# Performance work log

Hardware: AMD Instinct MI355X
Metric: run time of the kernel (lower is better)

Reference implementation:

```python
import jax, jax.numpy as jnp
import numpy as np

BN_EPS = 1e-5


def setup_inputs() -> dict:
    key = jax.random.key(0)
    ks = jax.random.split(key, 8)
    N, E, D, G, L = 50000, 800000, 128, 64, 4
    x = jax.random.normal(ks[0], (N, D), dtype=jnp.float32)
    edge_index = jax.random.randint(ks[1], (2, E), 0, N, dtype=jnp.int64)
    batch = jnp.sort(jax.random.randint(ks[2], (N,), 0, G, dtype=jnp.int64))
    sc = 1.0 / np.sqrt(D)
    W1 = jax.random.normal(ks[3], (L, D, D), dtype=jnp.float32) * sc
    b1 = jnp.zeros((L, D), dtype=jnp.float32)
    gamma = jnp.ones((L, D), dtype=jnp.float32)
    beta = jnp.zeros((L, D), dtype=jnp.float32)
    W2 = jax.random.normal(ks[4], (L, D, D), dtype=jnp.float32) * sc
    b2 = jnp.zeros((L, D), dtype=jnp.float32)
    return {"x": x, "edge_index": edge_index, "batch": batch,
            "W1": W1, "b1": b1, "gamma": gamma, "beta": beta,
            "W2": W2, "b2": b2}


def _segment_mean(vals, ids, num_segments):
    s = jax.ops.segment_sum(vals, ids, num_segments=num_segments)
    cnt = jax.ops.segment_sum(jnp.ones((vals.shape[0],), vals.dtype), ids,
                              num_segments=num_segments)
    return s / jnp.clip(cnt, 1.0)[:, None]


def reference(x, edge_index, batch, W1, b1, gamma, beta, W2, b2):
    N = x.shape[0]
    L = W1.shape[0]
    G = 64  # number of graphs
    src, dst = edge_index[0], edge_index[1]  # source_to_target flow
    # in-degree counts for scatter-mean (fixed across layers)
    deg = jax.ops.segment_sum(jnp.ones((src.shape[0],), x.dtype), dst,
                              num_segments=N)
    deg = jnp.clip(deg, 1.0)[:, None]
    h = x
    node_pool = jnp.zeros((N, W1.shape[2]), x.dtype)
    g_pool = jnp.zeros((G, W1.shape[2]), x.dtype)
    for l in range(L):
        # scatter-mean neighbor aggregation, GIN update with eps=0
        agg = jax.ops.segment_sum(h[src], dst, num_segments=N) / deg
        z = h + agg
        # MLP: Linear -> BatchNorm1d (batch stats) -> ReLU -> Linear
        z = z @ W1[l] + b1[l]
        mu = jnp.mean(z, axis=0)
        var = jnp.mean(jnp.square(z - mu), axis=0)  # biased, as in torch BN
        z = gamma[l] * (z - mu) * jax.lax.rsqrt(var + BN_EPS) + beta[l]
        z = jax.nn.relu(z)
        h = z @ W2[l] + b2[l]
        node_pool = node_pool + h
        g_pool = g_pool + _segment_mean(h, batch, G)
    return node_pool, g_pool
```

## Files before the change

kernel.cpp:

```cpp
#include <hip/hip_runtime.h>

#define D 128
#define GNUM 64
#define LNUM 4
#define BN_EPS 1e-5f
#define EPB 16384
#define SH_MAX 12544

typedef short bf16x8 __attribute__((ext_vector_type(8)));
typedef float f32x4 __attribute__((ext_vector_type(4)));
typedef unsigned short u16x8 __attribute__((ext_vector_type(8)));
typedef unsigned short u16x4 __attribute__((ext_vector_type(4)));

__device__ __forceinline__ float bf2f(unsigned short u) {
  union { unsigned int i; float f; } v; v.i = ((unsigned int)u) << 16; return v.f;
}
__device__ __forceinline__ unsigned short f2bf(float f) {
  union { float f; unsigned int i; } v; v.f = f;
  unsigned int b = v.i;
  return (unsigned short)((b + 0x7FFFu + ((b >> 16) & 1u)) >> 16);
}

__global__ __launch_bounds__(256) void k_hist(const int* __restrict__ ei, int E,
                                              int B, int nbin, int* __restrict__ hist) {
  __shared__ int lh[256];
  int b = blockIdx.x, tx = threadIdx.x;
  lh[tx] = 0;
  __syncthreads();
  int s = b * EPB, e = min(s + EPB, E);
  for (int j = s + tx; j < e; j += 256) atomicAdd(&lh[ei[(size_t)E + j] >> 8], 1);
  __syncthreads();
  if (tx < nbin) hist[tx * B + b] = lh[tx];
}

__global__ __launch_bounds__(1024) void k_hscan(const int* __restrict__ hist, int M,
                                                int* __restrict__ off,
                                                int* __restrict__ rowptr, int N, int E) {
  __shared__ int sh[SH_MAX];
  __shared__ int sh2[1024];
  int tx = threadIdx.x;
  int chunk = (M + 1023) / 1024;
  for (int i = 0; i < chunk; ++i) {
    int idx = tx * chunk + i;
    sh[idx] = (idx < M) ? hist[idx] : 0;
  }
  __syncthreads();
  int s = 0;
  for (int i = 0; i < chunk; ++i) s += sh[tx * chunk + i];
  sh2[tx] = s;
  __syncthreads();
  for (int o = 1; o < 1024; o <<= 1) {
    int u = (tx >= o) ? sh2[tx - o] : 0;
    __syncthreads();
    sh2[tx] += u;
    __syncthreads();
  }
  int run = (tx == 0) ? 0 : sh2[tx - 1];
  for (int i = 0; i < chunk; ++i) {
    int idx = tx * chunk + i;
    if (idx < M) { int v = sh[idx]; off[idx] = run; run += v; }
  }
  if (tx == 0) rowptr[N] = E;
}

__global__ __launch_bounds__(256) void k_scatter(const int* __restrict__ ei, int E,
                                                 int B, int nbin,
                                                 const int* __restrict__ off,
                                                 int2* __restrict__ sorted) {
  __shared__ int cur[256];
  int b = blockIdx.x, tx = threadIdx.x;
  if (tx < nbin) cur[tx] = off[tx * B + b];
  __syncthreads();
  int s = b * EPB, e = min(s + EPB, E);
  for (int j = s + tx; j < e; j += 256) {
    int d = ei[(size_t)E + j];
    int sc = ei[j];
    int p = atomicAdd(&cur[d >> 8], 1);
    sorted[p] = make_int2(d, sc);
  }
}

__global__ __launch_bounds__(256) void k_build(const int2* __restrict__ sorted,
                                               const int* __restrict__ off,
                                               int B, int nbin, int E, int N,
                                               int* __restrict__ rowptr,
                                               int* __restrict__ col) {
  __shared__ int cnt[256], excl[256], cur[256];
  int beta = blockIdx.x, tx = threadIdx.x;
  int s = off[beta * B];
  int e = (beta + 1 < nbin) ? off[(beta + 1) * B] : E;
  cnt[tx] = 0;
  __syncthreads();
  for (int j = s + tx; j < e; j += 256) atomicAdd(&cnt[sorted[j].x & 255], 1);
  __syncthreads();
  int v = cnt[tx];
  excl[tx] = v;
  __syncthreads();
  for (int o = 1; o < 256; o <<= 1) {
    int u = (tx >= o) ? excl[tx - o] : 0;
    __syncthreads();
    excl[tx] += u;
    __syncthreads();
  }
  int ex = excl[tx] - v;
  int n = beta * 256 + tx;
  if (n < N) rowptr[n] = s + ex;
  cur[tx] = s + ex;
  __syncthreads();
  for (int j = s + tx; j < e; j += 256) {
    int2 p = sorted[j];
    int q = atomicAdd(&cur[p.x & 255], 1);
    col[q] = p.y;
  }
}

__global__ void k_bounds(const int* __restrict__ batch, int N, int* __restrict__ bound) {
  int g = threadIdx.x;
  if (g > GNUM) return;
  int lo = 0, hi = N;
  while (lo < hi) { int mid = (lo + hi) >> 1; if (batch[mid] < g) lo = mid + 1; else hi = mid; }
  bound[g] = lo;
}

__global__ void k_prep_x(const float* __restrict__ x, unsigned short* __restrict__ hx, int total4) {
  int i = blockIdx.x * 256 + threadIdx.x;
  if (i < total4) {
    f32x4 v = ((const f32x4*)x)[i];
    u16x4 o; o[0] = f2bf(v[0]); o[1] = f2bf(v[1]); o[2] = f2bf(v[2]); o[3] = f2bf(v[3]);
    ((u16x4*)hx)[i] = o;
  }
}

__global__ __launch_bounds__(256) void k_prep_w(const float* __restrict__ W1,
                                                const float* __restrict__ W2,
                                                unsigned short* __restrict__ wt) {
  int l = blockIdx.x;
  const float* W = (l < LNUM) ? (W1 + (size_t)l * D * D) : (W2 + (size_t)(l - LNUM) * D * D);
  unsigned short* o = wt + (size_t)l * D * D;
#pragma unroll
  for (int i = 0; i < 64; ++i) {
    int idx = threadIdx.x + 256 * i;
    int k = idx >> 7, n = idx & 127;
    o[n * D + k] = f2bf(W[idx]);
  }
}

__global__ __launch_bounds__(256) void k_layer1(const unsigned short* __restrict__ hin,
                                                const int* __restrict__ rowptr,
                                                const int* __restrict__ col,
                                                const unsigned short* __restrict__ wt,
                                                const float* __restrict__ bias,
                                                unsigned short* __restrict__ t,
                                                float* __restrict__ partials, int N) {
  __shared__ union { unsigned short wl[D * D]; float out[64 * D]; } uB;
  __shared__ float red[2 * 8 * D];
  int tx = threadIdx.x;
  int r0 = blockIdx.x * 64;
  const u16x8* wg = (const u16x8*)wt;
#pragma unroll
  for (int i = 0; i < 8; ++i) {
    int cid = tx + 256 * i;
    int row = cid >> 4, c16 = cid & 15;
    u16x8 v = wg[cid];
    *(u16x8*)((char*)uB.wl + row * 256 + ((c16 * 16) ^ ((row & 7) << 4))) = v;
  }
  int l = tx & 63, w = tx >> 6;
  int lm = l & 15, lg = l >> 4;
  int row = 16 * w + lm;
  int n = r0 + row;
  const u16x8* h8 = (const u16x8*)hin;
  f32x4 sA[4] = {{0.f,0.f,0.f,0.f},{0.f,0.f,0.f,0.f},{0.f,0.f,0.f,0.f},{0.f,0.f,0.f,0.f}};
  f32x4 sB[4] = {{0.f,0.f,0.f,0.f},{0.f,0.f,0.f,0.f},{0.f,0.f,0.f,0.f},{0.f,0.f,0.f,0.f}};
  int e0 = 0, e1 = 0;
  if (n < N) { e0 = rowptr[n]; e1 = rowptr[n + 1]; }
  int j = e0;
  for (; j + 1 < e1; j += 2) {
    size_t c0 = (size_t)col[j] * 16 + lg;
    size_t c1 = (size_t)col[j + 1] * 16 + lg;
    u16x8 v00 = h8[c0];      u16x8 v01 = h8[c0 + 4];
    u16x8 v02 = h8[c0 + 8];  u16x8 v03 = h8[c0 + 12];
    u16x8 v10 = h8[c1];      u16x8 v11 = h8[c1 + 4];
    u16x8 v12 = h8[c1 + 8];  u16x8 v13 = h8[c1 + 12];
#pragma unroll
    for (int k = 0; k < 4; ++k) {
      sA[0][k] += bf2f(v00[k]) + bf2f(v10[k]);
      sB[0][k] += bf2f(v00[4 + k]) + bf2f(v10[4 + k]);
      sA[1][k] += bf2f(v01[k]) + bf2f(v11[k]);
      sB[1][k] += bf2f(v01[4 + k]) + bf2f(v11[4 + k]);
      sA[2][k] += bf2f(v02[k]) + bf2f(v12[k]);
      sB[2][k] += bf2f(v02[4 + k]) + bf2f(v12[4 + k]);
      sA[3][k] += bf2f(v03[k]) + bf2f(v13[k]);
      sB[3][k] += bf2f(v03[4 + k]) + bf2f(v13[4 + k]);
    }
  }
  if (j < e1) {
    size_t c0 = (size_t)col[j] * 16 + lg;
    u16x8 v00 = h8[c0];      u16x8 v01 = h8[c0 + 4];
    u16x8 v02 = h8[c0 + 8];  u16x8 v03 = h8[c0 + 12];
#pragma unroll
    for (int k = 0; k < 4; ++k) {
      sA[0][k] += bf2f(v00[k]);  sB[0][k] += bf2f(v00[4 + k]);
      sA[1][k] += bf2f(v01[k]);  sB[1][k] += bf2f(v01[4 + k]);
      sA[2][k] += bf2f(v02[k]);  sB[2][k] += bf2f(v02[4 + k]);
      sA[3][k] += bf2f(v03[k]);  sB[3][k] += bf2f(v03[4 + k]);
    }
  }
  bf16x8 af[4];
  if (n < N) {
    float inv = (e1 > e0) ? 1.f / (float)(e1 - e0) : 0.f;
#pragma unroll
    for (int kt = 0; kt < 4; ++kt) {
      u16x8 hv = h8[(size_t)n * 16 + kt * 4 + lg];
      u16x8 o;
#pragma unroll
      for (int k = 0; k < 4; ++k) {
        o[k] = f2bf(bf2f(hv[k]) + sA[kt][k] * inv);
        o[4 + k] = f2bf(bf2f(hv[4 + k]) + sB[kt][k] * inv);
      }
      af[kt] = *(bf16x8*)&o;
    }
  } else {
#pragma unroll
    for (int kt = 0; kt < 4; ++kt) af[kt] = (bf16x8){0,0,0,0,0,0,0,0};
  }
  __syncthreads();
  f32x4 acc[8];
#pragma unroll
  for (int cc = 0; cc < 8; ++cc) { float bv = bias[cc * 16 + lm]; acc[cc] = (f32x4){bv, bv, bv, bv}; }
#pragma unroll
  for (int kt = 0; kt < 4; ++kt) {
    int koff = kt * 64 + lg * 16;
#pragma unroll
    for (int cc = 0; cc < 8; ++cc) {
      int nn = cc * 16 + lm;
      bf16x8 bfr = *(const bf16x8*)((const char*)uB.wl + nn * 256 + (koff ^ ((nn & 7) << 4)));
      acc[cc] = __builtin_amdgcn_mfma_f32_16x16x32_bf16(af[kt], bfr, acc[cc], 0, 0, 0);
    }
  }
  __syncthreads();
#pragma unroll
  for (int cc = 0; cc < 8; ++cc)
#pragma unroll
    for (int r = 0; r < 4; ++r)
      uB.out[(16 * w + 4 * lg + r) * D + cc * 16 + lm] = acc[cc][r];
  __syncthreads();
  int tc = tx & 31, tr = tx >> 5;
  f32x4 s = {0.f, 0.f, 0.f, 0.f}, q = {0.f, 0.f, 0.f, 0.f};
#pragma unroll
  for (int i = 0; i < 8; ++i) {
    int rr = i * 8 + tr;
    f32x4 v = *(f32x4*)&uB.out[rr * D + tc * 4];
    u16x4 o; o[0] = f2bf(v[0]); o[1] = f2bf(v[1]); o[2] = f2bf(v[2]); o[3] = f2bf(v[3]);
    *(u16x4*)(t + (size_t)(r0 + rr) * D + tc * 4) = o;
    if (r0 + rr < N) { s += v; q += v * v; }
  }
  *(f32x4*)&red[tr * D + tc * 4] = s;
  *(f32x4*)&red[8 * D + tr * D + tc * 4] = q;
  __syncthreads();
  int colx = tx & 127, which = tx >> 7;
  float S = 0.f;
#pragma unroll
  for (int jj = 0; jj < 8; ++jj) S += red[which * 8 * D + jj * D + colx];
  partials[(size_t)blockIdx.x * 256 + tx] = S;
}

__global__ __launch_bounds__(256) void k_red1(const float* __restrict__ partials, int NB,
                                              float* __restrict__ partial2) {
  int tx = threadIdx.x;
  float S = 0.f;
  for (int b = blockIdx.x; b < NB; b += 64) S += partials[(size_t)b * 256 + tx];
  partial2[(size_t)blockIdx.x * 256 + tx] = S;
}

__global__ __launch_bounds__(256) void k_finalize(const float* __restrict__ partial2,
                                                  const float* __restrict__ gamma,
                                                  const float* __restrict__ beta,
                                                  float* __restrict__ stats, int N) {
  __shared__ float sh[256];
  int tx = threadIdx.x;
  float S = 0.f;
#pragma unroll 8
  for (int b = 0; b < 64; ++b) S += partial2[(size_t)b * 256 + tx];
  sh[tx] = S;
  __syncthreads();
  if (tx < D) {
    float mu = sh[tx] / (float)N;
    float var = sh[D + tx] / (float)N - mu * mu;
    float rstd = rsqrtf(fmaxf(var, 0.f) + BN_EPS);
    float A = gamma[tx] * rstd;
    stats[tx] = A;
    stats[D + tx] = beta[tx] - mu * A;
  }
}

__device__ __forceinline__ void gemm2_core(const unsigned short* t,
                                           const unsigned short* wt,
                                           const float* bias, const float* stats,
                                           unsigned short* at, unsigned short* wl,
                                           float* outbuf, int r0) {
  int tx = threadIdx.x;
  const u16x8* tg = (const u16x8*)(t + (size_t)r0 * D);
#pragma unroll
  for (int i = 0; i < 4; ++i) {
    int cid = tx + 256 * i;
    int row = cid >> 4, c16 = cid & 15;
    u16x8 v = tg[cid];
    int c0 = c16 * 8;
    f32x4 a0 = *(const f32x4*)&stats[c0];
    f32x4 a1 = *(const f32x4*)&stats[c0 + 4];
    f32x4 b0 = *(const f32x4*)&stats[D + c0];
    f32x4 b1v = *(const f32x4*)&stats[D + c0 + 4];
    u16x8 o;
    o[0] = f2bf(fmaxf(bf2f(v[0]) * a0[0] + b0[0], 0.f));
    o[1] = f2bf(fmaxf(bf2f(v[1]) * a0[1] + b0[1], 0.f));
    o[2] = f2bf(fmaxf(bf2f(v[2]) * a0[2] + b0[2], 0.f));
    o[3] = f2bf(fmaxf(bf2f(v[3]) * a0[3] + b0[3], 0.f));
    o[4] = f2bf(fmaxf(bf2f(v[4]) * a1[0] + b1v[0], 0.f));
    o[5] = f2bf(fmaxf(bf2f(v[5]) * a1[1] + b1v[1], 0.f));
    o[6] = f2bf(fmaxf(bf2f(v[6]) * a1[2] + b1v[2], 0.f));
    o[7] = f2bf(fmaxf(bf2f(v[7]) * a1[3] + b1v[3], 0.f));
    *(u16x8*)((char*)at + row * 256 + ((c16 * 16) ^ ((row & 7) << 4))) = o;
  }
  const u16x8* wg = (const u16x8*)wt;
#pragma unroll
  for (int i = 0; i < 8; ++i) {
    int cid = tx + 256 * i;
    int row = cid >> 4, c16 = cid & 15;
    u16x8 v = wg[cid];
    *(u16x8*)((char*)wl + row * 256 + ((c16 * 16) ^ ((row & 7) << 4))) = v;
  }
  __syncthreads();
  int l = tx & 63, w = tx >> 6;
  int lm = l & 15, lg = l >> 4;
  f32x4 acc[8];
#pragma unroll
  for (int c = 0; c < 8; ++c) { float bv = bias[c * 16 + lm]; acc[c] = (f32x4){bv, bv, bv, bv}; }
  int arow = 16 * w + lm;
  const char* ab = (const char*)at + arow * 256;
  int aswz = (arow & 7) << 4;
#pragma unroll
  for (int kt = 0; kt < 4; ++kt) {
    int koff = kt * 64 + lg * 16;
    bf16x8 af = *(const bf16x8*)(ab + (koff ^ aswz));
#pragma unroll
    for (int c = 0; c < 8; ++c) {
      int n = c * 16 + lm;
      bf16x8 bfr = *(const bf16x8*)((const char*)wl + n * 256 + (koff ^ ((n & 7) << 4)));
      acc[c] = __builtin_amdgcn_mfma_f32_16x16x32_bf16(af, bfr, acc[c], 0, 0, 0);
    }
  }
  __syncthreads();
#pragma unroll
  for (int c = 0; c < 8; ++c)
#pragma unroll
    for (int r = 0; r < 4; ++r)
      outbuf[(16 * w + 4 * lg + r) * D + c * 16 + lm] = acc[c][r];
  __syncthreads();
}

__global__ __launch_bounds__(256) void k_gemm2(const unsigned short* __restrict__ t,
                                               const unsigned short* __restrict__ wt,
                                               const float* __restrict__ bias,
                                               const float* __restrict__ stats,
                                               unsigned short* __restrict__ h, int N) {
  __shared__ unsigned short at[64 * D];
  __shared__ union { unsigned short wl[D * D]; float out[64 * D]; } uB;
  int tx = threadIdx.x;
  int r0 = blockIdx.x * 64;
  gemm2_core(t, wt, bias, stats, at, uB.wl, uB.out, r0);
  int tc = tx & 31, tr = tx >> 5;
#pragma unroll
  for (int i = 0; i < 8; ++i) {
    int row = i * 8 + tr;
    int gr = r0 + row;
    if (gr < N) {
      f32x4 v = *(f32x4*)&uB.out[row * D + tc * 4];
      u16x4 hb; hb[0] = f2bf(v[0]); hb[1] = f2bf(v[1]); hb[2] = f2bf(v[2]); hb[3] = f2bf(v[3]);
      *(u16x4*)(h + (size_t)gr * D + tc * 4) = hb;
    }
  }
}

__global__ __launch_bounds__(256) void k_gemm2_last(const unsigned short* __restrict__ t,
                                                    const unsigned short* __restrict__ wt,
                                                    const float* __restrict__ bias,
                                                    const float* __restrict__ stats,
                                                    const unsigned short* __restrict__ h0,
                                                    const unsigned short* __restrict__ h1,
                                                    const unsigned short* __restrict__ h2,
                                                    float* __restrict__ np, int N) {
  __shared__ unsigned short at[64 * D];
  __shared__ union { unsigned short wl[D * D]; float out[64 * D]; } uB;
  int tx = threadIdx.x;
  int r0 = blockIdx.x * 64;
  gemm2_core(t, wt, bias, stats, at, uB.wl, uB.out, r0);
  int tc = tx & 31, tr = tx >> 5;
#pragma unroll
  for (int i = 0; i < 8; ++i) {
    int row = i * 8 + tr;
    int gr = r0 + row;
    if (gr < N) {
      f32x4 v = *(f32x4*)&uB.out[row * D + tc * 4];
      size_t o4 = (size_t)gr * D + tc * 4;
      u16x4 a = *(const u16x4*)(h0 + o4);
      u16x4 b = *(const u16x4*)(h1 + o4);
      u16x4 cc = *(const u16x4*)(h2 + o4);
      f32x4 o;
#pragma unroll
      for (int k = 0; k < 4; ++k)
        o[k] = v[k] + (bf2f(a[k]) + bf2f(b[k])) + bf2f(cc[k]);
      *(f32x4*)(np + o4) = o;
    }
  }
}

__global__ __launch_bounds__(256) void k_gpool(const float* __restrict__ np,
                                               const int* __restrict__ bound,
                                               float* __restrict__ gp) {
  __shared__ float red[8 * D];
  int g = blockIdx.x;
  int s = bound[g], e = bound[g + 1];
  int tc = threadIdx.x & 31, tr = threadIdx.x >> 5;
  f32x4 a = {0.f, 0.f, 0.f, 0.f};
  for (int r = s + tr; r < e; r += 8)
    a += *(const f32x4*)(np + (size_t)r * D + tc * 4);
  *(f32x4*)&red[tr * D + tc * 4] = a;
  __syncthreads();
  if (threadIdx.x < D) {
    float v = 0.f;
#pragma unroll
    for (int j = 0; j < 8; ++j) v += red[j * D + threadIdx.x];
    float c = (float)(e - s);
    gp[(size_t)g * D + threadIdx.x] = v / fmaxf(c, 1.f);
  }
}

extern "C" void kernel_launch(void* const* d_in, const int* in_sizes, int n_in,
                              void* d_out, int out_size, void* d_ws,
                              size_t ws_size, hipStream_t stream) {
  const float* x = (const float*)d_in[0];
  const int* ei = (const int*)d_in[1];
  const int* batch = (const int*)d_in[2];
  const float* W1 = (const float*)d_in[3];
  const float* b1 = (const float*)d_in[4];
  const float* gamma = (const float*)d_in[5];
  const float* beta = (const float*)d_in[6];
  const float* W2 = (const float*)d_in[7];
  const float* b2 = (const float*)d_in[8];
  int N = in_sizes[0] / D;
  int E = in_sizes[1] / 2;
  int Npad = (N + 63) & ~63;
  int gb = Npad / 64;
  int B = (E + EPB - 1) / EPB;
  int nbin = (N + 255) / 256;
  int M = nbin * B;

  float* out = (float*)d_out;
  float* node_pool = out;
  float* g_pool = out + (size_t)N * D;

  char* wp = (char*)d_ws;
  unsigned short* hx = (unsigned short*)wp;   wp += (size_t)Npad * D * 2;
  unsigned short* t = (unsigned short*)wp;    wp += (size_t)Npad * D * 2;
  unsigned short* hbuf[3];
  for (int l = 0; l < 3; ++l) { hbuf[l] = (unsigned short*)wp; wp += (size_t)Npad * D * 2; }
  unsigned short* wt = (unsigned short*)wp;   wp += (size_t)8 * D * D * 2;
  float* partials = (float*)wp;               wp += (size_t)gb * 256 * 4;
  float* partial2 = (float*)wp;               wp += (size_t)64 * 256 * 4;
  float* stats = (float*)wp;                  wp += (size_t)2 * D * 4;
  int* bound = (int*)wp;                      wp += (size_t)(GNUM + 4) * 4;
  int* rowptr = (int*)wp;                     wp += (size_t)(N + 1) * 4;
  int* hist = (int*)wp;                       wp += (size_t)SH_MAX * 4;
  int* off = (int*)wp;                        wp += (size_t)SH_MAX * 4;
  int* col = (int*)wp;                        wp += (size_t)E * 4;
  int2* sorted = (int2*)wp;                   wp += (size_t)E * 8;

  k_prep_w<<<8, 256, 0, stream>>>(W1, W2, wt);
  k_prep_x<<<(N * 32 + 255) / 256, 256, 0, stream>>>(x, hx, N * 32);
  k_hist<<<B, 256, 0, stream>>>(ei, E, B, nbin, hist);
  k_hscan<<<1, 1024, 0, stream>>>(hist, M, off, rowptr, N, E);
  k_scatter<<<B, 256, 0, stream>>>(ei, E, B, nbin, off, sorted);
  k_build<<<nbin, 256, 0, stream>>>(sorted, off, B, nbin, E, N, rowptr, col);
  k_bounds<<<1, 128, 0, stream>>>(batch, N, bound);

  for (int ll = 0; ll < LNUM; ++ll) {
    const unsigned short* hin = (ll == 0) ? hx : hbuf[ll - 1];
    k_layer1<<<gb, 256, 0, stream>>>(hin, rowptr, col, wt + (size_t)ll * D * D,
                                     b1 + (size_t)ll * D, t, partials, N);
    k_red1<<<64, 256, 0, stream>>>(partials, gb, partial2);
    k_finalize<<<1, 256, 0, stream>>>(partial2, gamma + (size_t)ll * D,
                                      beta + (size_t)ll * D, stats, N);
    if (ll < LNUM - 1) {
      k_gemm2<<<gb, 256, 0, stream>>>(t, wt + (size_t)(LNUM + ll) * D * D,
                                      b2 + (size_t)ll * D, stats, hbuf[ll], N);
    } else {
      k_gemm2_last<<<gb, 256, 0, stream>>>(t, wt + (size_t)(LNUM + ll) * D * D,
                                           b2 + (size_t)ll * D, stats,
                                           hbuf[0], hbuf[1], hbuf[2], node_pool, N);
    }
  }
  k_gpool<<<GNUM, 256, 0, stream>>>(node_pool, bound, g_pool);
}
```

Baseline: 428.0 us.

## Sort rows by in-degree within each tile to balance gather work across lanes

```diff
diff --git a/kernel.cpp b/kernel.cpp
--- a/kernel.cpp
+++ b/kernel.cpp
@@ -122,6 +122,24 @@
   bound[g] = lo;
 }
 
+__global__ __launch_bounds__(64) void k_perm(const int* __restrict__ rowptr, int N,
+                                             int* __restrict__ perm) {
+  __shared__ int degs[64];
+  int r0 = blockIdx.x * 64;
+  int i = threadIdx.x;
+  int n = r0 + i;
+  int d = (n < N) ? (rowptr[n + 1] - rowptr[n]) : -1;
+  degs[i] = d;
+  __syncthreads();
+  int rank = 0;
+#pragma unroll
+  for (int j = 0; j < 64; ++j) {
+    int dj = degs[j];
+    if (dj < d || (dj == d && j < i)) ++rank;
+  }
+  perm[r0 + rank] = i;
+}
+
 __global__ void k_prep_x(const float* __restrict__ x, unsigned short* __restrict__ hx, int total4) {
   int i = blockIdx.x * 256 + threadIdx.x;
   if (i < total4) {
@@ -148,6 +166,7 @@
 __global__ __launch_bounds__(256) void k_layer1(const unsigned short* __restrict__ hin,
                                                 const int* __restrict__ rowptr,
                                                 const int* __restrict__ col,
+                                                const int* __restrict__ perm,
                                                 const unsigned short* __restrict__ wt,
                                                 const float* __restrict__ bias,
                                                 unsigned short* __restrict__ t,
@@ -166,43 +185,48 @@
   }
   int l = tx & 63, w = tx >> 6;
   int lm = l & 15, lg = l >> 4;
-  int row = 16 * w + lm;
-  int n = r0 + row;
+  int lr = perm[r0 + 16 * w + lm];
+  int pr0 = perm[r0 + 16 * w + 4 * lg + 0];
+  int pr1 = perm[r0 + 16 * w + 4 * lg + 1];
+  int pr2 = perm[r0 + 16 * w + 4 * lg + 2];
+  int pr3 = perm[r0 + 16 * w + 4 * lg + 3];
+  int n = r0 + lr;
   const u16x8* h8 = (const u16x8*)hin;
   f32x4 sA[4] = {{0.f,0.f,0.f,0.f},{0.f,0.f,0.f,0.f},{0.f,0.f,0.f,0.f},{0.f,0.f,0.f,0.f}};
   f32x4 sB[4] = {{0.f,0.f,0.f,0.f},{0.f,0.f,0.f,0.f},{0.f,0.f,0.f,0.f},{0.f,0.f,0.f,0.f}};
   int e0 = 0, e1 = 0;
   if (n < N) { e0 = rowptr[n]; e1 = rowptr[n + 1]; }
   int j = e0;
-  for (; j + 1 < e1; j += 2) {
-    size_t c0 = (size_t)col[j] * 16 + lg;
-    size_t c1 = (size_t)col[j + 1] * 16 + lg;
-    u16x8 v00 = h8[c0];      u16x8 v01 = h8[c0 + 4];
-    u16x8 v02 = h8[c0 + 8];  u16x8 v03 = h8[c0 + 12];
-    u16x8 v10 = h8[c1];      u16x8 v11 = h8[c1 + 4];
-    u16x8 v12 = h8[c1 + 8];  u16x8 v13 = h8[c1 + 12];
+  for (; j + 3 < e1; j += 4) {
+    size_t a0i = (size_t)col[j] * 16 + lg;
+    size_t a1i = (size_t)col[j + 1] * 16 + lg;
+    size_t a2i = (size_t)col[j + 2] * 16 + lg;
+    size_t a3i = (size_t)col[j + 3] * 16 + lg;
+    u16x8 u00 = h8[a0i], u01 = h8[a0i + 4], u02 = h8[a0i + 8], u03 = h8[a0i + 12];
+    u16x8 u10 = h8[a1i], u11 = h8[a1i + 4], u12 = h8[a1i + 8], u13 = h8[a1i + 12];
+    u16x8 u20 = h8[a2i], u21 = h8[a2i + 4], u22 = h8[a2i + 8], u23 = h8[a2i + 12];
+    u16x8 u30 = h8[a3i], u31 = h8[a3i + 4], u32 = h8[a3i + 8], u33 = h8[a3i + 12];
 #pragma unroll
     for (int k = 0; k < 4; ++k) {
-      sA[0][k] += bf2f(v00[k]) + bf2f(v10[k]);
-      sB[0][k] += bf2f(v00[4 + k]) + bf2f(v10[4 + k]);
-      sA[1][k] += bf2f(v01[k]) + bf2f(v11[k]);
-      sB[1][k] += bf2f(v01[4 + k]) + bf2f(v11[4 + k]);
-      sA[2][k] += bf2f(v02[k]) + bf2f(v12[k]);
-      sB[2][k] += bf2f(v02[4 + k]) + bf2f(v12[4 + k]);
-      sA[3][k] += bf2f(v03[k]) + bf2f(v13[k]);
-      sB[3][k] += bf2f(v03[4 + k]) + bf2f(v13[4 + k]);
-    }
-  }
-  if (j < e1) {
-    size_t c0 = (size_t)col[j] * 16 + lg;
-    u16x8 v00 = h8[c0];      u16x8 v01 = h8[c0 + 4];
-    u16x8 v02 = h8[c0 + 8];  u16x8 v03 = h8[c0 + 12];
+      sA[0][k] += (bf2f(u00[k]) + bf2f(u10[k])) + (bf2f(u20[k]) + bf2f(u30[k]));
+      sB[0][k] += (bf2f(u00[4+k]) + bf2f(u10[4+k])) + (bf2f(u20[4+k]) + bf2f(u30[4+k]));
+      sA[1][k] += (bf2f(u01[k]) + bf2f(u11[k])) + (bf2f(u21[k]) + bf2f(u31[k]));
+      sB[1][k] += (bf2f(u01[4+k]) + bf2f(u11[4+k])) + (bf2f(u21[4+k]) + bf2f(u31[4+k]));
+      sA[2][k] += (bf2f(u02[k]) + bf2f(u12[k])) + (bf2f(u22[k]) + bf2f(u32[k]));
+      sB[2][k] += (bf2f(u02[4+k]) + bf2f(u12[4+k])) + (bf2f(u22[4+k]) + bf2f(u32[4+k]));
+      sA[3][k] += (bf2f(u03[k]) + bf2f(u13[k])) + (bf2f(u23[k]) + bf2f(u33[k]));
+      sB[3][k] += (bf2f(u03[4+k]) + bf2f(u13[4+k])) + (bf2f(u23[4+k]) + bf2f(u33[4+k]));
+    }
+  }
+  for (; j < e1; ++j) {
+    size_t a0i = (size_t)col[j] * 16 + lg;
+    u16x8 u00 = h8[a0i], u01 = h8[a0i + 4], u02 = h8[a0i + 8], u03 = h8[a0i + 12];
 #pragma unroll
     for (int k = 0; k < 4; ++k) {
-      sA[0][k] += bf2f(v00[k]);  sB[0][k] += bf2f(v00[4 + k]);
-      sA[1][k] += bf2f(v01[k]);  sB[1][k] += bf2f(v01[4 + k]);
-      sA[2][k] += bf2f(v02[k]);  sB[2][k] += bf2f(v02[4 + k]);
-      sA[3][k] += bf2f(v03[k]);  sB[3][k] += bf2f(v03[4 + k]);
+      sA[0][k] += bf2f(u00[k]);  sB[0][k] += bf2f(u00[4+k]);
+      sA[1][k] += bf2f(u01[k]);  sB[1][k] += bf2f(u01[4+k]);
+      sA[2][k] += bf2f(u02[k]);  sB[2][k] += bf2f(u02[4+k]);
+      sA[3][k] += bf2f(u03[k]);  sB[3][k] += bf2f(u03[4+k]);
     }
   }
   bf16x8 af[4];
@@ -239,10 +263,12 @@
   }
   __syncthreads();
 #pragma unroll
-  for (int cc = 0; cc < 8; ++cc)
-#pragma unroll
-    for (int r = 0; r < 4; ++r)
-      uB.out[(16 * w + 4 * lg + r) * D + cc * 16 + lm] = acc[cc][r];
+  for (int cc = 0; cc < 8; ++cc) {
+    uB.out[pr0 * D + cc * 16 + lm] = acc[cc][0];
+    uB.out[pr1 * D + cc * 16 + lm] = acc[cc][1];
+    uB.out[pr2 * D + cc * 16 + lm] = acc[cc][2];
+    uB.out[pr3 * D + cc * 16 + lm] = acc[cc][3];
+  }
   __syncthreads();
   int tc = tx & 31, tr = tx >> 5;
   f32x4 s = {0.f, 0.f, 0.f, 0.f}, q = {0.f, 0.f, 0.f, 0.f};
@@ -470,6 +496,7 @@
   float* stats = (float*)wp;                  wp += (size_t)2 * D * 4;
   int* bound = (int*)wp;                      wp += (size_t)(GNUM + 4) * 4;
   int* rowptr = (int*)wp;                     wp += (size_t)(N + 1) * 4;
+  int* perm = (int*)wp;                       wp += (size_t)Npad * 4;
   int* hist = (int*)wp;                       wp += (size_t)SH_MAX * 4;
   int* off = (int*)wp;                        wp += (size_t)SH_MAX * 4;
   int* col = (int*)wp;                        wp += (size_t)E * 4;
@@ -481,11 +508,12 @@
   k_hscan<<<1, 1024, 0, stream>>>(hist, M, off, rowptr, N, E);
   k_scatter<<<B, 256, 0, stream>>>(ei, E, B, nbin, off, sorted);
   k_build<<<nbin, 256, 0, stream>>>(sorted, off, B, nbin, E, N, rowptr, col);
+  k_perm<<<gb, 64, 0, stream>>>(rowptr, N, perm);
   k_bounds<<<1, 128, 0, stream>>>(batch, N, bound);
 
   for (int ll = 0; ll < LNUM; ++ll) {
     const unsigned short* hin = (ll == 0) ? hx : hbuf[ll - 1];
-    k_layer1<<<gb, 256, 0, stream>>>(hin, rowptr, col, wt + (size_t)ll * D * D,
+    k_layer1<<<gb, 256, 0, stream>>>(hin, rowptr, col, perm, wt + (size_t)ll * D * D,
                                      b1 + (size_t)ll * D, t, partials, N);
     k_red1<<<64, 256, 0, stream>>>(partials, gb, partial2);
     k_finalize<<<1, 256, 0, stream>>>(partial2, gamma + (size_t)ll * D,
```

New measurement: 413.7 us. 1.03x faster.
